# Performance work log

Hardware: AMD Instinct MI355X
Metric: run time of the kernel (lower is better)

Reference implementation:

```python
import jax, jax.numpy as jnp
import numpy as np

N_NODES = 100000
DIM_IN = 128
DIM_OUT = 128
N_EDGES = 1600000
EPS = 0.0  # PyG GINConv default, non-trainable


def setup_inputs() -> dict:
    key = jax.random.key(0)
    k1, k2, k3, k4, k5, k6 = jax.random.split(key, 6)
    node_feature = jax.random.normal(k1, (N_NODES, DIM_IN), dtype=jnp.float32)
    edge_index = jax.random.randint(k2, (2, N_EDGES), 0, N_NODES, dtype=jnp.int64)
    s1 = 1.0 / np.sqrt(DIM_IN)
    s2 = 1.0 / np.sqrt(DIM_OUT)
    W1 = jax.random.uniform(k3, (DIM_IN, DIM_OUT), jnp.float32, -s1, s1)
    b1 = jax.random.uniform(k4, (DIM_OUT,), jnp.float32, -s1, s1)
    W2 = jax.random.uniform(k5, (DIM_OUT, DIM_OUT), jnp.float32, -s2, s2)
    b2 = jax.random.uniform(k6, (DIM_OUT,), jnp.float32, -s2, s2)
    return {"node_feature": node_feature, "edge_index": edge_index,
            "W1": W1, "b1": b1, "W2": W2, "b2": b2}


def reference(node_feature, edge_index, W1, b1, W2, b2):
    src, dst = edge_index[0], edge_index[1]
    # scatter-add neighbor aggregation: messages x_j = x[src] summed at dst
    agg = jax.ops.segment_sum(node_feature[src], dst, num_segments=N_NODES)  # [N, d]
    h = (1.0 + EPS) * node_feature + agg
    h = jax.nn.relu(h @ W1 + b1)
    return h @ W2 + b2
```

## Files before the change

### kernel.cpp

```cpp
#include <hip/hip_runtime.h>

#define NN 100000
#define D  128
#define NE 1600000

#define NBK2 782
#define CAP2 2816
#define EPB  8192
#define NFB  196

typedef __bf16 bf16x8 __attribute__((ext_vector_type(8)));
typedef __bf16 bf16x4 __attribute__((ext_vector_type(4)));
typedef __bf16 bf16x2 __attribute__((ext_vector_type(2)));
typedef float  f32x4  __attribute__((ext_vector_type(4)));

__global__ void xprep_kernel(const float* __restrict__ x, __bf16* __restrict__ xb) {
    int i = blockIdx.x * 256 + threadIdx.x;
    if (i < NN * 32) {
        float4 v = reinterpret_cast<const float4*>(x)[i];
        bf16x4 o = {(__bf16)v.x, (__bf16)v.y, (__bf16)v.z, (__bf16)v.w};
        reinterpret_cast<bf16x4*>(xb)[i] = o;
    }
}

__global__ void wprep_kernel(const float* __restrict__ W1, const float* __restrict__ W2,
                             __bf16* __restrict__ w1t, __bf16* __restrict__ w2t) {
    int i = blockIdx.x * 256 + threadIdx.x;
    if (i < 16384) {
        int c = i >> 7, k = i & 127;
        w1t[i] = (__bf16)W1[k * 128 + c];
    } else if (i < 32768) {
        int j = i - 16384;
        int c = j >> 7, k = j & 127;
        w2t[j] = (__bf16)W2[k * 128 + c];
    }
}

__global__ void zero_gcur_kernel(int* __restrict__ gcur) {
    int i = blockIdx.x * 256 + threadIdx.x;
    if (i < NBK2) gcur[i] = 0;
}

__global__ __launch_bounds__(512)
void fill2_kernel(const int* __restrict__ ei, int* __restrict__ gcur,
                  int* __restrict__ bedge) {
    __shared__ int            stage[EPB];
    __shared__ unsigned short bid16[EPB];
    __shared__ int            lofs[NBK2];
    __shared__ int            lpos[NBK2];
    __shared__ int            gbase[NBK2];
    __shared__ int            ssum[512];
    __shared__ int            tot;

    const int tid = threadIdx.x;
    const int e0  = blockIdx.x * EPB;

    for (int b = tid; b < NBK2; b += 512) lpos[b] = 0;
    __syncthreads();

    int eb[16], epk[16];
    #pragma unroll 16
    for (int k = 0; k < 16; ++k) {
        int e = e0 + k * 512 + tid;
        eb[k] = -1;
        if (e < NE) {
            int s = ei[e];
            int d = ei[NE + e];
            if ((unsigned)s < NN && (unsigned)d < NN) {
                eb[k]  = d >> 7;
                epk[k] = ((d & 127) << 17) | s;
                atomicAdd(&lpos[eb[k]], 1);
            }
        }
    }
    __syncthreads();

    int t2 = tid * 2;
    int c0 = (t2 < NBK2) ? lpos[t2] : 0;
    int c1 = (t2 + 1 < NBK2) ? lpos[t2 + 1] : 0;
    ssum[tid] = c0 + c1;
    __syncthreads();
    for (int off = 1; off < 512; off <<= 1) {
        int v = (tid >= off) ? ssum[tid - off] : 0;
        __syncthreads();
        ssum[tid] += v;
        __syncthreads();
    }
    int excl = ssum[tid] - (c0 + c1);
    if (t2 < NBK2) {
        lofs[t2] = excl;
        lpos[t2] = excl;
        if (c0) gbase[t2] = atomicAdd(&gcur[t2], c0);
    }
    if (t2 + 1 < NBK2) {
        lofs[t2 + 1] = excl + c0;
        lpos[t2 + 1] = excl + c0;
        if (c1) gbase[t2 + 1] = atomicAdd(&gcur[t2 + 1], c1);
    }
    if (tid == 511) tot = ssum[511];
    __syncthreads();

    #pragma unroll 16
    for (int k = 0; k < 16; ++k) {
        if (eb[k] >= 0) {
            int r = atomicAdd(&lpos[eb[k]], 1);
            stage[r] = epk[k];
            bid16[r] = (unsigned short)eb[k];
        }
    }
    __syncthreads();

    int T = tot;
    for (int i = tid; i < T; i += 512) {
        int b   = bid16[i];
        int pos = gbase[b] + (i - lofs[b]);
        if (pos < CAP2) bedge[b * CAP2 + pos] = stage[i];
    }
}

__global__ __launch_bounds__(512)
void gather2_kernel(const __bf16* __restrict__ xb, const int* __restrict__ gcur,
                    const int* __restrict__ bedge, __bf16* __restrict__ hb) {
    __shared__ int raw[CAP2];
    __shared__ int ent[CAP2];
    __shared__ int dlofs[129];
    __shared__ int dlpos[128];
    __shared__ int dscan[128];

    const int b   = blockIdx.x;
    const int tid = threadIdx.x;
    int cnt = gcur[b]; if (cnt > CAP2) cnt = CAP2;

    if (tid < 128) dlpos[tid] = 0;
    __syncthreads();
    for (int i = tid; i < cnt; i += 512) {
        int v = bedge[b * CAP2 + i];
        raw[i] = v;
        atomicAdd(&dlpos[v >> 17], 1);
    }
    __syncthreads();

    int c = (tid < 128) ? dlpos[tid] : 0;
    if (tid < 128) dscan[tid] = c;
    __syncthreads();
    for (int off = 1; off < 128; off <<= 1) {
        int v = (tid >= off && tid < 128) ? dscan[tid - off] : 0;
        __syncthreads();
        if (tid < 128) dscan[tid] += v;
        __syncthreads();
    }
    if (tid < 128) {
        dlofs[tid + 1] = dscan[tid];
        if (tid == 0) dlofs[0] = 0;
        dlpos[tid] = dscan[tid] - c;
    }
    __syncthreads();
    for (int i = tid; i < cnt; i += 512) {
        int v = raw[i];
        int r = atomicAdd(&dlpos[v >> 17], 1);
        ent[r] = v & 0x1FFFF;
    }
    __syncthreads();

    const int wave = tid >> 6, lane = tid & 63;
    const bf16x2* xv2 = reinterpret_cast<const bf16x2*>(xb);
    for (int nl = wave; nl < 128; nl += 8) {
        int node = b * 128 + nl;
        if (node >= NN) continue;
        int beg = dlofs[nl], end = dlofs[nl + 1];
        bf16x2 sv = xv2[(size_t)node * 64 + lane];
        float a0 = (float)sv[0], a1 = (float)sv[1];
        float b0 = 0.f, b1 = 0.f, c0f = 0.f, c1f = 0.f, d0 = 0.f, d1 = 0.f;
        int j = beg;
        for (; j + 4 <= end; j += 4) {
            int s0 = ent[j], s1 = ent[j + 1], s2 = ent[j + 2], s3 = ent[j + 3];
            bf16x2 v0 = xv2[(size_t)s0 * 64 + lane];
            bf16x2 v1 = xv2[(size_t)s1 * 64 + lane];
            bf16x2 v2 = xv2[(size_t)s2 * 64 + lane];
            bf16x2 v3 = xv2[(size_t)s3 * 64 + lane];
            a0  += (float)v0[0]; a1  += (float)v0[1];
            b0  += (float)v1[0]; b1  += (float)v1[1];
            c0f += (float)v2[0]; c1f += (float)v2[1];
            d0  += (float)v3[0]; d1  += (float)v3[1];
        }
        for (; j < end; ++j) {
            int s0 = ent[j];
            bf16x2 v0 = xv2[(size_t)s0 * 64 + lane];
            a0 += (float)v0[0]; a1 += (float)v0[1];
        }
        a0 += b0 + c0f + d0;
        a1 += b1 + c1f + d1;
        bf16x2 o = {(__bf16)a0, (__bf16)a1};
        reinterpret_cast<bf16x2*>(hb)[(size_t)node * 64 + lane] = o;
    }
}

__global__ __launch_bounds__(256)
void mlp_mfma_kernel(const __bf16* __restrict__ hb,
                     const __bf16* __restrict__ w1t,
                     const __bf16* __restrict__ w2t,
                     const float* __restrict__ b1,
                     const float* __restrict__ b2,
                     float* __restrict__ out) {
    __shared__ __align__(16) unsigned char sh_h[64 * 256];
    __shared__ __align__(16) unsigned char sh_w[128 * 256];

    const int tid   = threadIdx.x;
    const int wv    = tid >> 6;
    const int lane  = tid & 63;
    const int l15   = lane & 15;
    const int kbyte = (lane >> 4) * 16;
    const int row0  = blockIdx.x * 64;

    for (int c = tid; c < 1024; c += 256) {
        int r = c >> 4, s = c & 15;
        int grow = row0 + r;
        int4 val = make_int4(0, 0, 0, 0);
        if (grow < NN) val = *reinterpret_cast<const int4*>(hb + (size_t)grow * 128 + s * 8);
        *reinterpret_cast<int4*>(sh_h + r * 256 + ((s * 16) ^ ((r & 7) << 4))) = val;
    }
    for (int c = tid; c < 2048; c += 256) {
        int r = c >> 4, s = c & 15;
        int4 val = *reinterpret_cast<const int4*>(w1t + r * 128 + s * 8);
        *reinterpret_cast<int4*>(sh_w + r * 256 + ((s * 16) ^ ((r & 7) << 4))) = val;
    }
    __syncthreads();

    bf16x8 bf1[2][4];
    #pragma unroll
    for (int nn = 0; nn < 2; ++nn) {
        int col = wv * 32 + nn * 16 + l15;
        #pragma unroll
        for (int ks = 0; ks < 4; ++ks)
            bf1[nn][ks] = *reinterpret_cast<const bf16x8*>(
                sh_w + col * 256 + ((ks * 64 + kbyte) ^ ((col & 7) << 4)));
    }

    f32x4 acc[4][2];
    #pragma unroll
    for (int m = 0; m < 4; ++m) {
        acc[m][0] = f32x4{0.f, 0.f, 0.f, 0.f};
        acc[m][1] = f32x4{0.f, 0.f, 0.f, 0.f};
        int row = m * 16 + l15;
        bf16x8 af[4];
        #pragma unroll
        for (int ks = 0; ks < 4; ++ks)
            af[ks] = *reinterpret_cast<const bf16x8*>(
                sh_h + row * 256 + ((ks * 64 + kbyte) ^ ((row & 7) << 4)));
        #pragma unroll
        for (int ks = 0; ks < 4; ++ks) {
            acc[m][0] = __builtin_amdgcn_mfma_f32_16x16x32_bf16(af[ks], bf1[0][ks], acc[m][0], 0, 0, 0);
            acc[m][1] = __builtin_amdgcn_mfma_f32_16x16x32_bf16(af[ks], bf1[1][ks], acc[m][1], 0, 0, 0);
        }
    }

    float bias1a = b1[wv * 32 + l15];
    float bias1b = b1[wv * 32 + 16 + l15];

    __syncthreads();

    #pragma unroll
    for (int m = 0; m < 4; ++m) {
        #pragma unroll
        for (int nn = 0; nn < 2; ++nn) {
            int col = wv * 32 + nn * 16 + l15;
            float bb = nn ? bias1b : bias1a;
            #pragma unroll
            for (int j = 0; j < 4; ++j) {
                int row = m * 16 + (lane >> 4) * 4 + j;
                float v = fmaxf(acc[m][nn][j] + bb, 0.f);
                *reinterpret_cast<__bf16*>(
                    sh_h + row * 256 + ((col * 2) ^ ((row & 7) << 4))) = (__bf16)v;
            }
        }
    }
    for (int c = tid; c < 2048; c += 256) {
        int r = c >> 4, s = c & 15;
        int4 val = *reinterpret_cast<const int4*>(w2t + r * 128 + s * 8);
        *reinterpret_cast<int4*>(sh_w + r * 256 + ((s * 16) ^ ((r & 7) << 4))) = val;
    }
    __syncthreads();

    bf16x8 bf2[2][4];
    #pragma unroll
    for (int nn = 0; nn < 2; ++nn) {
        int col = wv * 32 + nn * 16 + l15;
        #pragma unroll
        for (int ks = 0; ks < 4; ++ks)
            bf2[nn][ks] = *reinterpret_cast<const bf16x8*>(
                sh_w + col * 256 + ((ks * 64 + kbyte) ^ ((col & 7) << 4)));
    }

    f32x4 acc2[4][2];
    #pragma unroll
    for (int m = 0; m < 4; ++m) {
        acc2[m][0] = f32x4{0.f, 0.f, 0.f, 0.f};
        acc2[m][1] = f32x4{0.f, 0.f, 0.f, 0.f};
        int row = m * 16 + l15;
        bf16x8 af[4];
        #pragma unroll
        for (int ks = 0; ks < 4; ++ks)
            af[ks] = *reinterpret_cast<const bf16x8*>(
                sh_h + row * 256 + ((ks * 64 + kbyte) ^ ((row & 7) << 4)));
        #pragma unroll
        for (int ks = 0; ks < 4; ++ks) {
            acc2[m][0] = __builtin_amdgcn_mfma_f32_16x16x32_bf16(af[ks], bf2[0][ks], acc2[m][0], 0, 0, 0);
            acc2[m][1] = __builtin_amdgcn_mfma_f32_16x16x32_bf16(af[ks], bf2[1][ks], acc2[m][1], 0, 0, 0);
        }
    }

    float bias2a = b2[wv * 32 + l15];
    float bias2b = b2[wv * 32 + 16 + l15];
    #pragma unroll
    for (int m = 0; m < 4; ++m) {
        #pragma unroll
        for (int nn = 0; nn < 2; ++nn) {
            int col = wv * 32 + nn * 16 + l15;
            float bb = nn ? bias2b : bias2a;
            #pragma unroll
            for (int j = 0; j < 4; ++j) {
                int row = row0 + m * 16 + (lane >> 4) * 4 + j;
                if (row < NN) out[(size_t)row * 128 + col] = acc2[m][nn][j] + bb;
            }
        }
    }
}

extern "C" void kernel_launch(void* const* d_in, const int* in_sizes, int n_in,
                              void* d_out, int out_size, void* d_ws, size_t ws_size,
                              hipStream_t stream) {
    const float* x  = (const float*)d_in[0];
    const int*   ei = (const int*)d_in[1];
    const float* W1 = (const float*)d_in[2];
    const float* b1 = (const float*)d_in[3];
    const float* W2 = (const float*)d_in[4];
    const float* b2 = (const float*)d_in[5];
    float* out = (float*)d_out;

    int* gcur  = (int*)d_ws;
    int* bedge = gcur + NBK2;
    size_t int_end = (size_t)(NBK2 + (size_t)NBK2 * CAP2) * 4;
    size_t bf_off  = (int_end + 255) & ~(size_t)255;
    __bf16* xb  = (__bf16*)((char*)d_ws + bf_off);
    __bf16* hb  = xb + (size_t)NN * D;
    __bf16* w1t = hb + (size_t)NN * D;
    __bf16* w2t = w1t + D * D;

    xprep_kernel<<<(NN * 32 + 255) / 256, 256, 0, stream>>>(x, xb);
    wprep_kernel<<<128, 256, 0, stream>>>(W1, W2, w1t, w2t);
    zero_gcur_kernel<<<(NBK2 + 255) / 256, 256, 0, stream>>>(gcur);

    fill2_kernel<<<NFB, 512, 0, stream>>>(ei, gcur, bedge);
    gather2_kernel<<<NBK2, 512, 0, stream>>>(xb, gcur, bedge, hb);

    mlp_mfma_kernel<<<(NN + 63) / 64, 256, 0, stream>>>(hb, w1t, w2t, b1, b2, out);
}
```

Measured before the change: 134.9 us.

## Split gather blocks into two halves and use 8-byte half-wave row loads

The gather kernel now launches two 256-thread blocks per 128-node bucket. Each block reads the whole bucket edge list but keeps only the edges for its own 64 destination nodes, which cuts LDS use (no raw copy) and should raise occupancy. In the accumulation loop each half-wave loads a full 128-element row as bf16x4 and handles a different edge, with a cross-half shuffle reduction at the end. The cost is reading bedge twice per block and a cap of ENTCAP entries per half, which could drop edges if a half exceeds 2048.

```diff
diff --git a/kernel.cpp b/kernel.cpp
--- a/kernel.cpp
+++ b/kernel.cpp
@@ -8,10 +8,10 @@
 #define CAP2 2816
 #define EPB  8192
 #define NFB  196
+#define ENTCAP 2048
 
 typedef __bf16 bf16x8 __attribute__((ext_vector_type(8)));
 typedef __bf16 bf16x4 __attribute__((ext_vector_type(4)));
-typedef __bf16 bf16x2 __attribute__((ext_vector_type(2)));
 typedef float  f32x4  __attribute__((ext_vector_type(4)));
 
 __global__ void xprep_kernel(const float* __restrict__ x, __bf16* __restrict__ xb) {
@@ -118,80 +118,104 @@
     }
 }
 
-__global__ __launch_bounds__(512)
-void gather2_kernel(const __bf16* __restrict__ xb, const int* __restrict__ gcur,
+__global__ __launch_bounds__(256)
+void gather3_kernel(const __bf16* __restrict__ xb, const int* __restrict__ gcur,
                     const int* __restrict__ bedge, __bf16* __restrict__ hb) {
-    __shared__ int raw[CAP2];
-    __shared__ int ent[CAP2];
-    __shared__ int dlofs[129];
-    __shared__ int dlpos[128];
-    __shared__ int dscan[128];
-
-    const int b   = blockIdx.x;
-    const int tid = threadIdx.x;
+    __shared__ int ent[ENTCAP];
+    __shared__ int c64[64], ofs[65], cur[64], scn[64];
+
+    const int b    = blockIdx.x >> 1;
+    const int half = blockIdx.x & 1;
+    const int tid  = threadIdx.x;
+
     int cnt = gcur[b]; if (cnt > CAP2) cnt = CAP2;
-
-    if (tid < 128) dlpos[tid] = 0;
-    __syncthreads();
-    for (int i = tid; i < cnt; i += 512) {
-        int v = bedge[b * CAP2 + i];
-        raw[i] = v;
-        atomicAdd(&dlpos[v >> 17], 1);
-    }
-    __syncthreads();
-
-    int c = (tid < 128) ? dlpos[tid] : 0;
-    if (tid < 128) dscan[tid] = c;
-    __syncthreads();
-    for (int off = 1; off < 128; off <<= 1) {
-        int v = (tid >= off && tid < 128) ? dscan[tid - off] : 0;
+    const int base = b * CAP2;
+
+    if (tid < 64) c64[tid] = 0;
+    __syncthreads();
+
+    for (int i = tid; i < cnt; i += 256) {
+        int v  = bedge[base + i];
+        int dl = v >> 17;
+        if ((dl >> 6) == half) atomicAdd(&c64[dl & 63], 1);
+    }
+    __syncthreads();
+
+    if (tid < 64) scn[tid] = c64[tid];
+    __syncthreads();
+    #pragma unroll
+    for (int off = 1; off < 64; off <<= 1) {
+        int v = (tid >= off && tid < 64) ? scn[tid - off] : 0;
         __syncthreads();
-        if (tid < 128) dscan[tid] += v;
+        if (tid < 64) scn[tid] += v;
         __syncthreads();
     }
-    if (tid < 128) {
-        dlofs[tid + 1] = dscan[tid];
-        if (tid == 0) dlofs[0] = 0;
-        dlpos[tid] = dscan[tid] - c;
-    }
-    __syncthreads();
-    for (int i = tid; i < cnt; i += 512) {
-        int v = raw[i];
-        int r = atomicAdd(&dlpos[v >> 17], 1);
-        ent[r] = v & 0x1FFFF;
-    }
-    __syncthreads();
-
-    const int wave = tid >> 6, lane = tid & 63;
-    const bf16x2* xv2 = reinterpret_cast<const bf16x2*>(xb);
-    for (int nl = wave; nl < 128; nl += 8) {
-        int node = b * 128 + nl;
+    if (tid < 64) {
+        ofs[tid + 1] = scn[tid];
+        if (tid == 0) ofs[0] = 0;
+        cur[tid] = scn[tid] - c64[tid];
+    }
+    __syncthreads();
+
+    for (int i = tid; i < cnt; i += 256) {
+        int v  = bedge[base + i];
+        int dl = v >> 17;
+        if ((dl >> 6) == half) {
+            int r = atomicAdd(&cur[dl & 63], 1);
+            if (r < ENTCAP) ent[r] = v & 0x1FFFF;
+        }
+    }
+    __syncthreads();
+
+    const int wave   = tid >> 6;
+    const int lane   = tid & 63;
+    const int half32 = lane >> 5;
+    const int l31    = lane & 31;
+    const bf16x4* xv4 = reinterpret_cast<const bf16x4*>(xb);
+
+    for (int q = wave; q < 64; q += 4) {
+        int node = b * 128 + half * 64 + q;
         if (node >= NN) continue;
-        int beg = dlofs[nl], end = dlofs[nl + 1];
-        bf16x2 sv = xv2[(size_t)node * 64 + lane];
-        float a0 = (float)sv[0], a1 = (float)sv[1];
-        float b0 = 0.f, b1 = 0.f, c0f = 0.f, c1f = 0.f, d0 = 0.f, d1 = 0.f;
+        int beg = ofs[q], end = ofs[q + 1];
+        if (beg > ENTCAP) beg = ENTCAP;
+        if (end > ENTCAP) end = ENTCAP;
+
+        float a0 = 0.f, a1 = 0.f, a2 = 0.f, a3 = 0.f;
+        float b0 = 0.f, b1 = 0.f, b2f = 0.f, b3 = 0.f;
         int j = beg;
         for (; j + 4 <= end; j += 4) {
-            int s0 = ent[j], s1 = ent[j + 1], s2 = ent[j + 2], s3 = ent[j + 3];
-            bf16x2 v0 = xv2[(size_t)s0 * 64 + lane];
-            bf16x2 v1 = xv2[(size_t)s1 * 64 + lane];
-            bf16x2 v2 = xv2[(size_t)s2 * 64 + lane];
-            bf16x2 v3 = xv2[(size_t)s3 * 64 + lane];
-            a0  += (float)v0[0]; a1  += (float)v0[1];
-            b0  += (float)v1[0]; b1  += (float)v1[1];
-            c0f += (float)v2[0]; c1f += (float)v2[1];
-            d0  += (float)v3[0]; d1  += (float)v3[1];
-        }
-        for (; j < end; ++j) {
+            int s0 = ent[j + half32];
+            int s1 = ent[j + 2 + half32];
+            bf16x4 v0 = xv4[(size_t)s0 * 32 + l31];
+            bf16x4 v1 = xv4[(size_t)s1 * 32 + l31];
+            a0 += (float)v0[0]; a1 += (float)v0[1];
+            a2 += (float)v0[2]; a3 += (float)v0[3];
+            b0 += (float)v1[0]; b1 += (float)v1[1];
+            b2f += (float)v1[2]; b3 += (float)v1[3];
+        }
+        if (j + 2 <= end) {
+            int s0 = ent[j + half32];
+            bf16x4 v0 = xv4[(size_t)s0 * 32 + l31];
+            a0 += (float)v0[0]; a1 += (float)v0[1];
+            a2 += (float)v0[2]; a3 += (float)v0[3];
+            j += 2;
+        }
+        if (j < end && half32 == 0) {
             int s0 = ent[j];
-            bf16x2 v0 = xv2[(size_t)s0 * 64 + lane];
+            bf16x4 v0 = xv4[(size_t)s0 * 32 + l31];
             a0 += (float)v0[0]; a1 += (float)v0[1];
-        }
-        a0 += b0 + c0f + d0;
-        a1 += b1 + c1f + d1;
-        bf16x2 o = {(__bf16)a0, (__bf16)a1};
-        reinterpret_cast<bf16x2*>(hb)[(size_t)node * 64 + lane] = o;
+            a2 += (float)v0[2]; a3 += (float)v0[3];
+        }
+        a0 += b0; a1 += b1; a2 += b2f; a3 += b3;
+        a0 += __shfl_xor(a0, 32); a1 += __shfl_xor(a1, 32);
+        a2 += __shfl_xor(a2, 32); a3 += __shfl_xor(a3, 32);
+
+        if (half32 == 0) {
+            bf16x4 sv = xv4[(size_t)node * 32 + l31];
+            bf16x4 o = {(__bf16)(a0 + (float)sv[0]), (__bf16)(a1 + (float)sv[1]),
+                        (__bf16)(a2 + (float)sv[2]), (__bf16)(a3 + (float)sv[3])};
+            reinterpret_cast<bf16x4*>(hb)[(size_t)node * 32 + l31] = o;
+        }
     }
 }
 
@@ -351,7 +375,7 @@
     zero_gcur_kernel<<<(NBK2 + 255) / 256, 256, 0, stream>>>(gcur);
 
     fill2_kernel<<<NFB, 512, 0, stream>>>(ei, gcur, bedge);
-    gather2_kernel<<<NBK2, 512, 0, stream>>>(xb, gcur, bedge, hb);
+    gather3_kernel<<<NBK2 * 2, 256, 0, stream>>>(xb, gcur, bedge, hb);
 
     mlp_mfma_kernel<<<(NN + 63) / 64, 256, 0, stream>>>(hb, w1t, w2t, b1, b2, out);
 }
```

After: 134.9 us. Within noise of the previous version (+0.0%).
